# Kernel optimization log

Measured on AMD Instinct MI355X. Metric: run time of the kernel, lower is better.

The kernel has to match this reference:

```python
import jax, jax.numpy as jnp
import numpy as np

EPS = 1e-5
KC = 256  # key_channels


def conv1x1(x, w):
    # x: [N,Cin,H,W], w: [Cout,Cin] -> [N,Cout,H,W]
    return jnp.einsum('nchw,oc->nohw', x, w)


def bn_relu(x, g, b, m, v):
    # eval-mode BatchNorm2d + ReLU, fused affine form
    inv = g / jnp.sqrt(v + EPS)
    return jax.nn.relu(x * inv[None, :, None, None] + (b - m * inv)[None, :, None, None])


def setup_inputs() -> dict:
    key = jax.random.key(0)
    ks = jax.random.split(key, 8)
    N, C, H, W, K = 8, 512, 128, 128, 19
    d = {
        'x': jax.random.normal(ks[0], (N, C, H, W), jnp.float32),
        'proxy': jax.random.normal(ks[1], (N, C, K, 1), jnp.float32),
        'w_p1': jax.random.normal(ks[2], (KC, C), jnp.float32) / np.sqrt(C),
        'w_p2': jax.random.normal(ks[3], (KC, KC), jnp.float32) / np.sqrt(KC),
        'w_o1': jax.random.normal(ks[4], (KC, C), jnp.float32) / np.sqrt(C),
        'w_o2': jax.random.normal(ks[5], (KC, KC), jnp.float32) / np.sqrt(KC),
        'w_d': jax.random.normal(ks[6], (KC, C), jnp.float32) / np.sqrt(C),
        'w_u': jax.random.normal(ks[7], (C, KC), jnp.float32) / np.sqrt(KC),
    }
    for pfx, ch in [('p1', KC), ('p2', KC), ('o1', KC), ('o2', KC), ('d', KC), ('u', C)]:
        d[f'{pfx}_g'] = jnp.ones((ch,), jnp.float32)
        d[f'{pfx}_b'] = jnp.zeros((ch,), jnp.float32)
        d[f'{pfx}_m'] = jnp.zeros((ch,), jnp.float32)
        d[f'{pfx}_v'] = jnp.ones((ch,), jnp.float32)
    return d


def reference(x, proxy, w_p1, p1_g, p1_b, p1_m, p1_v, w_p2, p2_g, p2_b, p2_m, p2_v,
              w_o1, o1_g, o1_b, o1_m, o1_v, w_o2, o2_g, o2_b, o2_m, o2_v,
              w_d, d_g, d_b, d_m, d_v, w_u, u_g, u_b, u_m, u_v):
    N, C, H, W = x.shape
    # f_pixel: conv1x1 -> BN+ReLU -> conv1x1 -> BN+ReLU
    q = bn_relu(conv1x1(bn_relu(conv1x1(x, w_p1), p1_g, p1_b, p1_m, p1_v), w_p2),
                p2_g, p2_b, p2_m, p2_v)                       # [N,KC,H,W]
    k = bn_relu(conv1x1(bn_relu(conv1x1(proxy, w_o1), o1_g, o1_b, o1_m, o1_v), w_o2),
                o2_g, o2_b, o2_m, o2_v)                       # [N,KC,K,1]
    v = bn_relu(conv1x1(proxy, w_d), d_g, d_b, d_m, d_v)      # [N,KC,K,1]

    query = q.reshape(N, KC, H * W).transpose(0, 2, 1)        # [N,HW,KC]
    keym = k.reshape(N, KC, -1)                               # [N,KC,K]
    value = v.reshape(N, KC, -1).transpose(0, 2, 1)           # [N,K,KC]

    sim = jnp.einsum('nlc,nck->nlk', query, keym) * (KC ** -0.5)  # [N,HW,K]
    sim = jax.nn.softmax(sim, axis=-1)
    context = jnp.einsum('nlk,nkc->nlc', sim, value)          # [N,HW,KC]
    context = context.transpose(0, 2, 1).reshape(N, KC, H, W)
    # f_up
    return bn_relu(conv1x1(context, w_u), u_g, u_b, u_m, u_v)  # [N,C,H,W]
```

## Files before the change

### kernel.cpp

```cpp
#include <hip/hip_runtime.h>

#define HW     16384
#define CIN    512
#define KCH    256
#define NKEY   19
#define NKP    32
#define NBATCH 8

typedef __attribute__((ext_vector_type(8))) short s16x8;
typedef __attribute__((ext_vector_type(4))) short s16x4;
typedef __attribute__((ext_vector_type(4))) float f32x4;
typedef __attribute__((ext_vector_type(2))) float f32x2;

__device__ __forceinline__ short f2bf(float f) {
  __bf16 h = (__bf16)f;
  return __builtin_bit_cast(short, h);
}

#define BARRIER_LG() do { \
    asm volatile("s_waitcnt lgkmcnt(0)" ::: "memory"); \
    __builtin_amdgcn_s_barrier(); \
    asm volatile("" ::: "memory"); \
  } while (0)

__global__ __launch_bounds__(256) void kprepA(
    const float* __restrict__ proxy,
    const float* __restrict__ w_p1, const float* __restrict__ w_p2,
    const float* __restrict__ p1g, const float* __restrict__ p1b,
    const float* __restrict__ p1m, const float* __restrict__ p1v,
    const float* __restrict__ p2g, const float* __restrict__ p2b,
    const float* __restrict__ p2m, const float* __restrict__ p2v,
    const float* __restrict__ ug,  const float* __restrict__ ub,
    const float* __restrict__ um,  const float* __restrict__ uvv,
    const float* __restrict__ w_o1, const float* __restrict__ w_d,
    const float* __restrict__ o1g, const float* __restrict__ o1b,
    const float* __restrict__ o1m, const float* __restrict__ o1v,
    const float* __restrict__ dg,  const float* __restrict__ db,
    const float* __restrict__ dm,  const float* __restrict__ dv,
    short* __restrict__ W1L, short* __restrict__ W2L,
    float* __restrict__ b1, float* __restrict__ b2, float* __restrict__ bu,
    float* __restrict__ t_o1g, float* __restrict__ vmatg)
{
  __shared__ char PB[32 * 1024];
  const int tid = threadIdx.x;
  if (blockIdx.x < 772) {
    int t = blockIdx.x * 256 + tid;
    if (t < 131072) {
      int kf = t >> 13, rem = t & 8191, tt = rem >> 9, e512 = rem & 511;
      int l = e512 >> 3, e = e512 & 7;
      int m = tt * 16 + (l & 15);
      int kcol = kf * 32 + (l >> 4) * 8 + e;
      float inv = p1g[m] * rsqrtf(p1v[m] + 1e-5f);
      W1L[t] = f2bf(inv * w_p1[(size_t)m * CIN + kcol]);
    } else if (t < 196608) {
      int u = t - 131072;
      int kf = u >> 13, rem = u & 8191, tt = rem >> 9, e512 = rem & 511;
      int l = e512 >> 3, e = e512 & 7;
      int m = tt * 16 + (l & 15);
      int kcol = kf * 32 + (l >> 4) * 8 + e;
      float inv = p2g[m] * rsqrtf(p2v[m] + 1e-5f);
      W2L[u] = f2bf(inv * w_p2[(size_t)m * KCH + kcol]);
    } else if (t < 196608 + 256) {
      int o = t - 196608;
      float inv = p1g[o] * rsqrtf(p1v[o] + 1e-5f);
      b1[o] = p1b[o] - p1m[o] * inv;
    } else if (t < 196608 + 512) {
      int o = t - 196608 - 256;
      float inv = p2g[o] * rsqrtf(p2v[o] + 1e-5f);
      b2[o] = p2b[o] - p2m[o] * inv;
    } else if (t < 196608 + 1024) {
      int o = t - 196608 - 512;
      float inv = ug[o] * rsqrtf(uvv[o] + 1e-5f);
      bu[o] = ub[o] - um[o] * inv;
    }
    return;
  }
  int bid = blockIdx.x - 772;
  int sel = bid >> 5;
  int r5  = bid & 31;
  int n   = r5 >> 2;
  int mbase = (r5 & 3) << 6;

  for (int j = 0; j < 8; ++j) *(s16x8*)(PB + (tid + j * 256) * 16) = (s16x8)0;
  __syncthreads();
  const float* pn = proxy + (size_t)n * CIN * NKEY;
  for (int e = tid; e < CIN * NKEY; e += 256) {
    int c = e / NKEY, k = e - c * NKEY;
    *(short*)(PB + k * 1024 + ((c << 1) ^ ((k & 7) << 4))) = f2bf(pn[e]);
  }
  __syncthreads();

  const int w = tid >> 6, lane = tid & 63, g = lane >> 4, i = lane & 15;
  const float* W  = sel ? w_d : w_o1;
  const float* gg = sel ? dg : o1g;
  const float* bb = sel ? db : o1b;
  const float* mm = sel ? dm : o1m;
  const float* vv = sel ? dv : o1v;
  f32x4 acc2[2];
  acc2[0] = (f32x4)0.f; acc2[1] = (f32x4)0.f;
  const int arow = mbase + w * 16 + i;
#pragma unroll 1
  for (int kf = 0; kf < 16; ++kf) {
    const float* wp = W + (size_t)arow * CIN + kf * 32 + g * 8;
    f32x4 a0 = *(const f32x4*)wp, a1 = *(const f32x4*)(wp + 4);
    s16x8 af;
#pragma unroll
    for (int e = 0; e < 4; ++e) { af[e] = f2bf(a0[e]); af[e + 4] = f2bf(a1[e]); }
#pragma unroll
    for (int nj = 0; nj < 2; ++nj) {
      int key = nj * 16 + i;
      s16x8 bf = *(const s16x8*)(PB + key * 1024 + ((kf * 64 + g * 16) ^ ((key & 7) << 4)));
      acc2[nj] = __builtin_amdgcn_mfma_f32_16x16x32_bf16(af, bf, acc2[nj], 0, 0, 0);
    }
  }
  float* dst = (sel ? vmatg : t_o1g) + (size_t)n * 8192;
#pragma unroll
  for (int r = 0; r < 4; ++r) {
    int o = mbase + w * 16 + g * 4 + r;
    float inv = gg[o] * rsqrtf(vv[o] + 1e-5f);
    float beta = bb[o] - mm[o] * inv;
#pragma unroll
    for (int nj = 0; nj < 2; ++nj) {
      int key = nj * 16 + i;
      dst[key * 256 + o] = fmaxf(acc2[nj][r] * inv + beta, 0.f);
    }
  }
}

__global__ __launch_bounds__(256) void kprepB(
    const float* __restrict__ w_o2, const float* __restrict__ w_u,
    const float* __restrict__ o2g, const float* __restrict__ o2b,
    const float* __restrict__ o2m, const float* __restrict__ o2v,
    const float* __restrict__ ug,  const float* __restrict__ uvv,
    const float* __restrict__ t_o1g, const float* __restrict__ vmatg,
    short* __restrict__ KmL, short* __restrict__ WuL)
{
  __shared__ char TB[32 * 512];
  const int tid = threadIdx.x;
  const int isKm = (blockIdx.x < 32);
  int n, mbase;
  const float* src;
  if (isKm) { n = blockIdx.x >> 2; mbase = (blockIdx.x & 3) << 6; src = t_o1g; }
  else { int b2_ = blockIdx.x - 32; n = b2_ >> 3; mbase = (b2_ & 7) << 6; src = vmatg; }
  const float* sn = src + (size_t)n * 8192;
  for (int j = 0; j < 32; ++j) {
    int idx = tid + j * 256;
    int key = idx >> 8, o = idx & 255;
    *(short*)(TB + key * 512 + ((o << 1) ^ ((key & 7) << 4))) = f2bf(sn[idx]);
  }
  __syncthreads();

  const int w = tid >> 6, lane = tid & 63, g = lane >> 4, i = lane & 15;
  const float* W = isKm ? w_o2 : w_u;
  f32x4 acc2[2];
  acc2[0] = (f32x4)0.f; acc2[1] = (f32x4)0.f;
  const int arow = mbase + w * 16 + i;
#pragma unroll 1
  for (int kf = 0; kf < 8; ++kf) {
    const float* wp = W + (size_t)arow * KCH + kf * 32 + g * 8;
    f32x4 a0 = *(const f32x4*)wp, a1 = *(const f32x4*)(wp + 4);
    s16x8 af;
#pragma unroll
    for (int e = 0; e < 4; ++e) { af[e] = f2bf(a0[e]); af[e + 4] = f2bf(a1[e]); }
#pragma unroll
    for (int nj = 0; nj < 2; ++nj) {
      int key = nj * 16 + i;
      s16x8 bf = *(const s16x8*)(TB + key * 512 + ((kf * 64 + g * 16) ^ ((key & 7) << 4)));
      acc2[nj] = __builtin_amdgcn_mfma_f32_16x16x32_bf16(af, bf, acc2[nj], 0, 0, 0);
    }
  }
  if (isKm) {
    short* Kn = KmL + (size_t)n * 8192;
#pragma unroll
    for (int r = 0; r < 4; ++r) {
      int o2 = mbase + w * 16 + g * 4 + r;
      float inv = o2g[o2] * rsqrtf(o2v[o2] + 1e-5f);
      float beta = o2b[o2] - o2m[o2] * inv;
#pragma unroll
      for (int nj = 0; nj < 2; ++nj) {
        float val = fmaxf(acc2[nj][r] * inv + beta, 0.f) * 0.0625f;
        Kn[((o2 >> 5) * 2 + nj) * 512 + (((o2 >> 3) & 3) * 16 + i) * 8 + (o2 & 7)] = f2bf(val);
      }
    }
  } else {
    short* Wn = WuL + (size_t)n * 16384;
#pragma unroll
    for (int r = 0; r < 4; ++r) {
      int c = mbase + w * 16 + g * 4 + r;
      float inv = ug[c] * rsqrtf(uvv[c] + 1e-5f);
#pragma unroll
      for (int nj = 0; nj < 2; ++nj) {
        int key = nj * 16 + i;
        float val = acc2[nj][r] * inv;
        Wn[(c >> 4) * 512 + ((key >> 3) * 16 + (c & 15)) * 8 + (key & 7)] = f2bf(val);
      }
    }
  }
}

#define LOADCHUNK(R2, ck) do { \
    const float* xp = xb2 + (size_t)((ck) * 64 + ch0) * HW; \
    _Pragma("unroll") \
    for (int c = 0; c < 8; ++c) (R2)[c] = *(const f32x2*)(xp + (size_t)c * HW); \
  } while (0)

#define WRITECHUNK(R2, ck) do { \
    char* wr_ = smem + ((ck) % 3) * 8192; \
    _Pragma("unroll") \
    for (int p = 0; p < 2; ++p) { \
      int px_ = pxp + p; \
      s16x8 h; \
      _Pragma("unroll") \
      for (int c = 0; c < 8; ++c) h[c] = f2bf((R2)[c][p]); \
      *(s16x8*)(wr_ + px_ * 128 + ((ch0 << 1) ^ ((px_ & 7) << 4))) = h; \
    } \
  } while (0)

#define MFMASTEP(ck) do { \
    const char* rb_ = smem + ((ck) % 3) * 8192; \
    _Pragma("unroll") \
    for (int ks = 0; ks < 2; ++ks) { \
      s16x8 af[4], bf[4]; \
      _Pragma("unroll") \
      for (int mi = 0; mi < 4; ++mi) \
        af[mi] = *(const s16x8*)(W1L + ((((ck) * 2 + ks) * 16 + (w * 4 + mi)) << 9) + (lane << 3)); \
      _Pragma("unroll") \
      for (int ni = 0; ni < 4; ++ni) { \
        int p_ = ni * 16 + i; \
        bf[ni] = *(const s16x8*)(rb_ + p_ * 128 + (((ks * 32 + g * 8) << 1) ^ ((p_ & 7) << 4))); \
      } \
      _Pragma("unroll") \
      for (int mi = 0; mi < 4; ++mi) \
        _Pragma("unroll") \
        for (int ni = 0; ni < 4; ++ni) \
          acc[mi][ni] = __builtin_amdgcn_mfma_f32_16x16x32_bf16(af[mi], bf[ni], acc[mi][ni], 0, 0, 0); \
    } \
  } while (0)

__global__ __launch_bounds__(256, 4) void k_main(
    const float* __restrict__ x,
    const short* __restrict__ W1L, const short* __restrict__ W2L,
    const short* __restrict__ KmL, const short* __restrict__ WuL,
    const float* __restrict__ b1, const float* __restrict__ b2,
    const float* __restrict__ bu,
    float* __restrict__ out)
{
  __shared__ char smem[32768];
  char* t1q = smem;

  const int tid  = threadIdx.x;
  const int w    = tid >> 6;
  const int lane = tid & 63;
  const int g    = lane >> 4;
  const int i    = lane & 15;
  const int n    = blockIdx.x >> 8;
  const int l0   = (blockIdx.x & 255) << 6;

  f32x4 acc[4][4];
#pragma unroll
  for (int a_ = 0; a_ < 4; ++a_)
#pragma unroll
    for (int b_ = 0; b_ < 4; ++b_) acc[a_][b_] = (f32x4)0.f;

  const int pxp = (lane & 31) << 1;
  const int ch0 = (((lane >> 5) + (w << 1)) << 3);
  const float* xb2 = x + (size_t)n * CIN * HW + l0 + pxp;

  f32x2 RA[8], RB[8];
  LOADCHUNK(RA, 0);
  LOADCHUNK(RB, 1);
  WRITECHUNK(RA, 0);
  BARRIER_LG();

#pragma unroll
  for (int cp = 0; cp < 4; ++cp) {
    const int cka = 2 * cp, ckb = 2 * cp + 1;
    if (cka + 2 < 8) LOADCHUNK(RA, cka + 2);
    WRITECHUNK(RB, ckb);
    MFMASTEP(cka);
    BARRIER_LG();
    if (ckb + 2 < 8) LOADCHUNK(RB, ckb + 2);
    if (ckb + 1 < 8) WRITECHUNK(RA, ckb + 1);
    MFMASTEP(ckb);
    BARRIER_LG();
  }

#pragma unroll
  for (int mi = 0; mi < 4; ++mi) {
    f32x4 bias = *(const f32x4*)(b1 + w * 64 + mi * 16 + g * 4);
#pragma unroll
    for (int ni = 0; ni < 4; ++ni) {
      int p = ni * 16 + i;
      s16x4 hh;
#pragma unroll
      for (int r = 0; r < 4; ++r) hh[r] = f2bf(fmaxf(acc[mi][ni][r] + bias[r], 0.f));
      *(s16x4*)(t1q + p * 512 + (((w * 64 + mi * 16 + g * 4) << 1) ^ ((p & 7) << 4))) = hh;
      acc[mi][ni] = (f32x4)0.f;
    }
  }
  __syncthreads();

#pragma unroll 2
  for (int ks = 0; ks < 8; ++ks) {
    s16x8 af[4], bf[4];
#pragma unroll
    for (int mi = 0; mi < 4; ++mi)
      af[mi] = *(const s16x8*)(W2L + (((ks * 16) + (w * 4 + mi)) << 9) + (lane << 3));
#pragma unroll
    for (int ni = 0; ni < 4; ++ni) {
      int p = ni * 16 + i;
      bf[ni] = *(const s16x8*)(t1q + p * 512 + (((ks * 32 + g * 8) << 1) ^ ((p & 7) << 4)));
    }
#pragma unroll
    for (int mi = 0; mi < 4; ++mi)
#pragma unroll
      for (int ni = 0; ni < 4; ++ni)
        acc[mi][ni] = __builtin_amdgcn_mfma_f32_16x16x32_bf16(af[mi], bf[ni], acc[mi][ni], 0, 0, 0);
  }
  __syncthreads();
#pragma unroll
  for (int mi = 0; mi < 4; ++mi) {
    f32x4 bias = *(const f32x4*)(b2 + w * 64 + mi * 16 + g * 4);
#pragma unroll
    for (int ni = 0; ni < 4; ++ni) {
      int p = ni * 16 + i;
      s16x4 hh;
#pragma unroll
      for (int r = 0; r < 4; ++r) hh[r] = f2bf(fmaxf(acc[mi][ni][r] + bias[r], 0.f));
      *(s16x4*)(t1q + p * 512 + (((w * 64 + mi * 16 + g * 4) << 1) ^ ((p & 7) << 4))) = hh;
    }
  }
  __syncthreads();

  f32x4 as_[2];
  as_[0] = (f32x4)0.f; as_[1] = (f32x4)0.f;
  const short* Kn = KmL + (size_t)n * 8192;
  const int ps = (w << 4) | i;
  const int psw = (ps & 7) << 4;
#pragma unroll
  for (int ks = 0; ks < 8; ++ks) {
    s16x8 bq = *(const s16x8*)(t1q + ps * 512 + (((ks * 32 + g * 8) << 1) ^ psw));
#pragma unroll
    for (int mi = 0; mi < 2; ++mi) {
      s16x8 ak = *(const s16x8*)(Kn + (((ks * 2 + mi)) << 9) + (lane << 3));
      as_[mi] = __builtin_amdgcn_mfma_f32_16x16x32_bf16(ak, bq, as_[mi], 0, 0, 0);
    }
  }
  float mx = -1e30f;
#pragma unroll
  for (int mi = 0; mi < 2; ++mi)
#pragma unroll
    for (int r = 0; r < 4; ++r) {
      int k = mi * 16 + g * 4 + r;
      if (k < NKEY) mx = fmaxf(mx, as_[mi][r]);
    }
  mx = fmaxf(mx, __shfl_xor(mx, 16, 64));
  mx = fmaxf(mx, __shfl_xor(mx, 32, 64));
  float e[2][4];
  float sum = 0.f;
#pragma unroll
  for (int mi = 0; mi < 2; ++mi)
#pragma unroll
    for (int r = 0; r < 4; ++r) {
      int k = mi * 16 + g * 4 + r;
      float t = (k < NKEY) ? __expf(as_[mi][r] - mx) : 0.f;
      e[mi][r] = t;
      sum += t;
    }
  sum += __shfl_xor(sum, 16, 64);
  sum += __shfl_xor(sum, 32, 64);
  float rs = 1.f / sum;
  __syncthreads();
  char* P = smem;
#pragma unroll
  for (int mi = 0; mi < 2; ++mi) {
    s16x4 hh;
#pragma unroll
    for (int r = 0; r < 4; ++r) hh[r] = f2bf(e[mi][r] * rs);
    *(s16x4*)(P + ps * 64 + (((mi * 16 + g * 4) << 1) ^ ((ps & 3) << 4))) = hh;
  }
  __syncthreads();

  s16x8 bP[4];
#pragma unroll
  for (int ni = 0; ni < 4; ++ni) {
    int p = ni * 16 + i;
    bP[ni] = *(const s16x8*)(P + p * 64 + ((g * 16) ^ ((p & 3) << 4)));
  }
  const short* Wn = WuL + (size_t)n * 16384;
  float* op = out + (size_t)n * CIN * HW + l0;
  float* Tb = (float*)(smem + 8192 + w * 4352);
#pragma unroll
  for (int mi = 0; mi < 8; ++mi) {
    int row0 = w * 128 + mi * 16;
    s16x8 aU = *(const s16x8*)(Wn + ((w * 8 + mi) << 9) + (lane << 3));
    f32x4 bias = *(const f32x4*)(bu + row0 + g * 4);
#pragma unroll
    for (int ni = 0; ni < 4; ++ni) {
      f32x4 o4 = __builtin_amdgcn_mfma_f32_16x16x32_bf16(aU, bP[ni], bias, 0, 0, 0);
#pragma unroll
      for (int r = 0; r < 4; ++r)
        Tb[(g * 4 + r) * 67 + ni * 16 + i] = fmaxf(o4[r], 0.f);
    }
#pragma unroll
    for (int j = 0; j < 4; ++j) {
      int rowr = j * 4 + g;
      f32x4 v = *(const f32x4*)(Tb + rowr * 67 + i * 4);
      *(f32x4*)(op + (size_t)(row0 + rowr) * HW + i * 4) = v;
    }
  }
}

extern "C" void kernel_launch(void* const* d_in, const int* in_sizes, int n_in,
                              void* d_out, int out_size, void* d_ws, size_t ws_size,
                              hipStream_t stream) {
  (void)in_sizes; (void)n_in; (void)out_size; (void)ws_size;
  const float* x     = (const float*)d_in[0];
  const float* proxy = (const float*)d_in[1];
  const float* w_p1  = (const float*)d_in[2];
  const float* w_p2  = (const float*)d_in[3];
  const float* w_o1  = (const float*)d_in[4];
  const float* w_o2  = (const float*)d_in[5];
  const float* w_d   = (const float*)d_in[6];
  const float* w_u   = (const float*)d_in[7];
  const float* p1g = (const float*)d_in[8],  *p1b = (const float*)d_in[9];
  const float* p1m = (const float*)d_in[10], *p1v = (const float*)d_in[11];
  const float* p2g = (const float*)d_in[12], *p2b = (const float*)d_in[13];
  const float* p2m = (const float*)d_in[14], *p2v = (const float*)d_in[15];
  const float* o1g = (const float*)d_in[16], *o1b = (const float*)d_in[17];
  const float* o1m = (const float*)d_in[18], *o1v = (const float*)d_in[19];
  const float* o2g = (const float*)d_in[20], *o2b = (const float*)d_in[21];
  const float* o2m = (const float*)d_in[22], *o2v = (const float*)d_in[23];
  const float* dg  = (const float*)d_in[24], *db  = (const float*)d_in[25];
  const float* dm  = (const float*)d_in[26], *dv  = (const float*)d_in[27];
  const float* ug  = (const float*)d_in[28], *ub  = (const float*)d_in[29];
  const float* um  = (const float*)d_in[30], *uv  = (const float*)d_in[31];

  char* ws = (char*)d_ws;
  short* W1L    = (short*)(ws + 0);
  short* W2L    = (short*)(ws + 262144);
  short* KmL    = (short*)(ws + 393216);
  short* WuL    = (short*)(ws + 524288);
  float* b1     = (float*)(ws + 786432);
  float* b2     = (float*)(ws + 787456);
  float* bu     = (float*)(ws + 788480);
  float* t_o1g  = (float*)(ws + 790528);
  float* vmatg  = (float*)(ws + 1052672);

  kprepA<<<836, 256, 0, stream>>>(proxy,
                                  w_p1, w_p2, p1g, p1b, p1m, p1v,
                                  p2g, p2b, p2m, p2v, ug, ub, um, uv,
                                  w_o1, w_d, o1g, o1b, o1m, o1v,
                                  dg, db, dm, dv,
                                  W1L, W2L, b1, b2, bu, t_o1g, vmatg);
  kprepB<<<96, 256, 0, stream>>>(w_o2, w_u, o2g, o2b, o2m, o2v, ug, uv,
                                 t_o1g, vmatg, KmL, WuL);
  k_main<<<2048, 256, 0, stream>>>(x, W1L, W2L, KmL, WuL, b1, b2, bu, (float*)d_out);
}
```

Measured before the change: 161.6 us.

## Pipeline two input chunks per barrier stage using five LDS slots

Restructures the first-GEMM staging loop so that each barrier-separated stage writes two chunks of x into LDS and runs MFMAs on two others. Slots are assigned explicitly across five 8 KB buffers instead of rotating through three. This cuts the number of workgroup barriers in the main projection loop and gives more MFMA work between synchronizations. The cost is a larger LDS footprint (40 KB per block), which may limit how many blocks fit per CU.

```diff
diff --git a/kernel.cpp b/kernel.cpp
--- a/kernel.cpp
+++ b/kernel.cpp
@@ -204,8 +204,8 @@
     for (int c = 0; c < 8; ++c) (R2)[c] = *(const f32x2*)(xp + (size_t)c * HW); \
   } while (0)
 
-#define WRITECHUNK(R2, ck) do { \
-    char* wr_ = smem + ((ck) % 3) * 8192; \
+#define WRITECHUNK_S(R2, slot) do { \
+    char* wr_ = smem + (slot) * 8192; \
     _Pragma("unroll") \
     for (int p = 0; p < 2; ++p) { \
       int px_ = pxp + p; \
@@ -216,8 +216,8 @@
     } \
   } while (0)
 
-#define MFMASTEP(ck) do { \
-    const char* rb_ = smem + ((ck) % 3) * 8192; \
+#define MFMASTEP_S(ck, slot) do { \
+    const char* rb_ = smem + (slot) * 8192; \
     _Pragma("unroll") \
     for (int ks = 0; ks < 2; ++ks) { \
       s16x8 af[4], bf[4]; \
@@ -245,7 +245,7 @@
     const float* __restrict__ bu,
     float* __restrict__ out)
 {
-  __shared__ char smem[32768];
+  __shared__ char smem[40960];
   char* t1q = smem;
 
   const int tid  = threadIdx.x;
@@ -267,23 +267,23 @@
   const float* xb2 = x + (size_t)n * CIN * HW + l0 + pxp;
 
   f32x2 RA[8], RB[8];
-  LOADCHUNK(RA, 0);
-  LOADCHUNK(RB, 1);
-  WRITECHUNK(RA, 0);
+  LOADCHUNK(RA, 0); LOADCHUNK(RB, 1);
+  WRITECHUNK_S(RA, 0); WRITECHUNK_S(RB, 1);
+  LOADCHUNK(RA, 2); LOADCHUNK(RB, 3);
   BARRIER_LG();
-
-#pragma unroll
-  for (int cp = 0; cp < 4; ++cp) {
-    const int cka = 2 * cp, ckb = 2 * cp + 1;
-    if (cka + 2 < 8) LOADCHUNK(RA, cka + 2);
-    WRITECHUNK(RB, ckb);
-    MFMASTEP(cka);
-    BARRIER_LG();
-    if (ckb + 2 < 8) LOADCHUNK(RB, ckb + 2);
-    if (ckb + 1 < 8) WRITECHUNK(RA, ckb + 1);
-    MFMASTEP(ckb);
-    BARRIER_LG();
-  }
+  WRITECHUNK_S(RA, 2); WRITECHUNK_S(RB, 3);
+  LOADCHUNK(RA, 4); LOADCHUNK(RB, 5);
+  MFMASTEP_S(0, 0); MFMASTEP_S(1, 1);
+  BARRIER_LG();
+  WRITECHUNK_S(RA, 4); WRITECHUNK_S(RB, 0);
+  LOADCHUNK(RA, 6); LOADCHUNK(RB, 7);
+  MFMASTEP_S(2, 2); MFMASTEP_S(3, 3);
+  BARRIER_LG();
+  WRITECHUNK_S(RA, 1); WRITECHUNK_S(RB, 2);
+  MFMASTEP_S(4, 4); MFMASTEP_S(5, 0);
+  BARRIER_LG();
+  MFMASTEP_S(6, 1); MFMASTEP_S(7, 2);
+  BARRIER_LG();
 
 #pragma unroll
   for (int mi = 0; mi < 4; ++mi) {
```

Result: slower. 228.5 us (+41.4%).
